# Performance work log

Hardware: AMD Instinct MI355X
Metric: run time of the kernel (lower is better)

## Reference

```python
import jax, jax.numpy as jnp
import numpy as np

B, N, C, H = 4, 2048, 256, 16
D = C // H  # head dim = 16


def setup_inputs() -> dict:
    key = jax.random.key(0)
    k1, k2, k3 = jax.random.split(key, 3)
    x = jax.random.normal(k1, (B, N, C), dtype=jnp.float32)
    w_qkv = jax.random.normal(k2, (C, 3 * C), dtype=jnp.float32) * (C ** -0.5)
    b_qkv = jnp.zeros((3 * C,), dtype=jnp.float32)
    w_proj = jax.random.normal(k3, (C, C), dtype=jnp.float32) * (C ** -0.5)
    b_proj = jnp.zeros((C,), dtype=jnp.float32)
    return {"x": x, "w_qkv": w_qkv, "b_qkv": b_qkv, "w_proj": w_proj, "b_proj": b_proj}


def reference(x, w_qkv, b_qkv, w_proj, b_proj):
    b, n, c = x.shape
    qkv = x @ w_qkv + b_qkv                       # (B, N, 3C)
    qkv = qkv.reshape(b, n, 3, H, D)
    q = jnp.transpose(qkv[:, :, 0], (0, 2, 1, 3))  # (B, H, N, D)
    k = jnp.transpose(qkv[:, :, 1], (0, 2, 1, 3))
    v = jnp.transpose(qkv[:, :, 2], (0, 2, 1, 3))
    # NOTE: the original module applies NO 1/sqrt(d) scaling.
    attn = jnp.einsum('bhqd,bhkd->bhqk', q, k)     # (B, H, N, N)
    attn = jax.nn.softmax(attn, axis=-1)
    out = jnp.einsum('bhqk,bhkd->bhqd', attn, v)   # (B, H, N, D)
    out = jnp.transpose(out, (0, 2, 1, 3)).reshape(b, n, c)
    return out @ w_proj + b_proj
```

## Files before the change

kernel.cpp:

```cpp
#include <hip/hip_runtime.h>
#include <stdint.h>

typedef __attribute__((ext_vector_type(8))) short short8;
typedef __attribute__((ext_vector_type(4))) short short4v;
typedef __attribute__((ext_vector_type(4))) float float4v;
typedef __attribute__((ext_vector_type(16))) float float16v;
typedef __attribute__((ext_vector_type(4))) uint32_t uint4v;

__device__ __forceinline__ short f2bf(float f) {
    union { float f; uint32_t u; } v; v.f = f;
    uint32_t u = v.u;
    uint32_t r = (u + 0x7fffu + ((u >> 16) & 1u)) >> 16;
    return (short)r;
}

#if __has_builtin(__builtin_amdgcn_cvt_pk_bf16_f32)
typedef __bf16 bf16x2_t __attribute__((ext_vector_type(2)));
__device__ __forceinline__ uint32_t cvt_pk2(float a, float b) {
    union { bf16x2_t v; uint32_t u; } c;
    c.v = __builtin_amdgcn_cvt_pk_bf16_f32(a, b);
    return c.u;
}
#else
__device__ __forceinline__ uint32_t cvt_pk2(float a, float b) {
    union { float f; uint32_t u; } x, y; x.f = a; y.f = b;
    return ((x.u + 0x8000u) >> 16) | ((y.u + 0x8000u) & 0xFFFF0000u);
}
#endif

__device__ __forceinline__ void async_ld16(short* lds, const short* g) {
    __builtin_amdgcn_global_load_lds(
        (const __attribute__((address_space(1))) void*)g,
        (__attribute__((address_space(3))) void*)lds, 16, 0, 0);
}


__global__ __launch_bounds__(256) void cvtW_kernel(const float* __restrict__ wqkv,
                                                   const float* __restrict__ wproj,
                                                   const float* __restrict__ x,
                                                   short* __restrict__ outq,
                                                   short* __restrict__ outp,
                                                   short* __restrict__ xb) {
    int gid = blockIdx.x * 256 + threadIdx.x;
    if (gid < 262144) {
        const float* src = x + (size_t)gid * 8;
        float4 f0 = *(const float4*)src;
        float4 f1 = *(const float4*)(src + 4);
        uint4v u; u.x = cvt_pk2(f0.x, f0.y); u.y = cvt_pk2(f0.z, f0.w);
        u.z = cvt_pk2(f1.x, f1.y); u.w = cvt_pk2(f1.z, f1.w);
        *(uint4v*)(xb + (size_t)gid * 8) = u;
    } else {
        int idx = gid - 262144;
        if (idx < 196608) {
            int n = idx >> 8, k = idx & 255;
            outq[idx] = f2bf(wqkv[k * 768 + n]);
        } else {
            int i = idx - 196608;
            int n = i >> 8, k = i & 255;
            outp[i] = f2bf(wproj[k * 256 + n]);
        }
    }
}


template<int TM, int MODE>
__global__ __launch_bounds__(256) void gemm2_kernel(
    const short* __restrict__ A, const short* __restrict__ Bt,
    const float* __restrict__ bias,
    short* __restrict__ outQ, short* __restrict__ outK, short* __restrict__ outV,
    float* __restrict__ outP)
{
    const int K = 256;
    const int MI = TM / 32;
    int tid = threadIdx.x;
    int w = tid >> 6, lane = tid & 63;
    int wr = w >> 1, wc = w & 1;
    int quad = lane >> 4, lc = lane & 15;
    int m0 = blockIdx.x * TM, n0 = blockIdx.y * 128;

    __shared__ __align__(16) short As[TM * 64];
    __shared__ __align__(16) short Bs[128 * 64];

    float4v acc[MI][4];
    #pragma unroll
    for (int i = 0; i < MI; ++i)
        #pragma unroll
        for (int j = 0; j < 4; ++j) acc[i][j] = (float4v){0.f, 0.f, 0.f, 0.f};

    int l8 = lane >> 3, l7 = lane & 7;
    int scol = ((l7 ^ l8) * 8);

    for (int kt = 0; kt < 4; ++kt) {
        int c = kt * 64;
        __syncthreads();
        #pragma unroll
        for (int i = 0; i < TM / 32; ++i) {
            int row = i * 32 + w * 8 + l8;
            async_ld16(&As[row * 64 + l7 * 8],
                       A + (size_t)(m0 + row) * K + c + scol);
        }
        #pragma unroll
        for (int i = 0; i < 4; ++i) {
            int row = i * 32 + w * 8 + l8;
            async_ld16(&Bs[row * 64 + l7 * 8],
                       Bt + (size_t)(n0 + row) * K + c + scol);
        }
        __syncthreads();

        #pragma unroll
        for (int ks = 0; ks < 2; ++ks) {
            short8 af[MI], bf[4];
            #pragma unroll
            for (int i = 0; i < MI; ++i) {
                int r = wr * (TM / 2) + i * 16 + lc;
                af[i] = *(short8*)(&As[r * 64 + (((ks * 4 + quad) ^ (r & 7)) * 8)]);
            }
            #pragma unroll
            for (int j = 0; j < 4; ++j) {
                int r = wc * 64 + j * 16 + lc;
                bf[j] = *(short8*)(&Bs[r * 64 + (((ks * 4 + quad) ^ (r & 7)) * 8)]);
            }
            #pragma unroll
            for (int i = 0; i < MI; ++i)
                #pragma unroll
                for (int j = 0; j < 4; ++j)
                    acc[i][j] = __builtin_amdgcn_mfma_f32_16x16x32_bf16(af[i], bf[j], acc[i][j], 0, 0, 0);
        }
    }

    #pragma unroll
    for (int i = 0; i < MI; ++i) {
        #pragma unroll
        for (int j = 0; j < 4; ++j) {
            int cg = n0 + wc * 64 + j * 16 + lc;
            float bv = bias[cg];
            #pragma unroll
            for (int r = 0; r < 4; ++r) {
                int rg = m0 + wr * (TM / 2) + i * 16 + quad * 4 + r;
                float val = acc[i][j][r] + bv;
                if (MODE == 0) {
                    int sq = cg >> 8, rem = cg & 255, h = rem >> 4, d = rem & 15;
                    int b = rg >> 11, n = rg & 2047;
                    if (sq == 0) val *= 1.4426950408889634f;
                    short* dst = (sq == 0) ? outQ : ((sq == 1) ? outK : outV);
                    dst[((((size_t)b * 16 + h) * 2048 + n) << 4) + d] = f2bf(val);
                } else {
                    outP[(size_t)rg * 256 + cg] = val;
                }
            }
        }
    }
}


__global__ __launch_bounds__(256) void attn_kernel(
    const short* __restrict__ Q, const short* __restrict__ Kp, const short* __restrict__ V,
    short* __restrict__ Out)
{
    const int N = 2048;
    int bh = blockIdx.y;
    int b = bh >> 4, h = bh & 15;
    int tid = threadIdx.x;
    int wave = tid >> 6, lane = tid & 63;
    int m = lane & 31, hi = lane >> 5;
    int qbase = blockIdx.x * 128 + wave * 32;

    const short* Qh = Q + (size_t)bh * N * 16;
    const short* Kh = Kp + (size_t)bh * N * 16;
    const short* Vh = V + (size_t)bh * N * 16;

    __shared__ __align__(16) short Vt[32][264];

    for (int idx = tid; idx < 16 * 264; idx += 256) {
        int row = 16 + idx / 264;
        int col = idx - (row - 16) * 264;
        Vt[row][col] = (row == 16) ? (short)0x3F80 : (short)0;
    }

    short8 qf = *(const short8*)(Qh + (size_t)(qbase + m) * 16 + hi * 8);

    float16v Oacc, zf;
    #pragma unroll
    for (int j = 0; j < 16; ++j) { Oacc[j] = 0.f; zf[j] = 0.f; }

    int sd = tid & 15, sa = tid >> 4;
    int kb = ((sa & 1) << 3) | (((sa >> 1) & 1) << 2) | ((sa >> 2) << 4);

    short4v vpack[4];
    #pragma unroll
    for (int cc = 0; cc < 4; ++cc) {
        const short* vp = Vh + (size_t)(cc * 64 + kb) * 16 + sd;
        vpack[cc].x = vp[0]; vpack[cc].y = vp[16];
        vpack[cc].z = vp[32]; vpack[cc].w = vp[48];
    }

    short8 kf1 = *(const short8*)(Kh + (size_t)m * 16 + hi * 8);
    short8 kf2 = *(const short8*)(Kh + (size_t)(32 + m) * 16 + hi * 8);

    for (int sc = 0; sc < N; sc += 256) {
        __syncthreads();
        #pragma unroll
        for (int cc = 0; cc < 4; ++cc)
            *(short4v*)(&Vt[sd][cc * 64 + sa * 4]) = vpack[cc];
        if (sc + 256 < N) {
            #pragma unroll
            for (int cc = 0; cc < 4; ++cc) {
                const short* vp = Vh + (size_t)(sc + 256 + cc * 64 + kb) * 16 + sd;
                vpack[cc].x = vp[0]; vpack[cc].y = vp[16];
                vpack[cc].z = vp[32]; vpack[cc].w = vp[48];
            }
        }
        __syncthreads();

        #pragma unroll
        for (int it = 0; it < 4; ++it) {
            int c = sc + it * 64;
            int cn = (c + 64) & (N - 1);

            float16v S1 = __builtin_amdgcn_mfma_f32_32x32x16_bf16(kf1, qf, zf, 0, 0, 0);
            float16v S2 = __builtin_amdgcn_mfma_f32_32x32x16_bf16(kf2, qf, zf, 0, 0, 0);

            kf1 = *(const short8*)(Kh + (size_t)(cn + m) * 16 + hi * 8);
            kf2 = *(const short8*)(Kh + (size_t)(cn + 32 + m) * 16 + hi * 8);

            union { uint4v u; short8 s; } pA, pB, pC, pD;
            pA.u = (uint4v){
                cvt_pk2(__builtin_amdgcn_exp2f(S1[0]), __builtin_amdgcn_exp2f(S1[1])),
                cvt_pk2(__builtin_amdgcn_exp2f(S1[2]), __builtin_amdgcn_exp2f(S1[3])),
                cvt_pk2(__builtin_amdgcn_exp2f(S1[4]), __builtin_amdgcn_exp2f(S1[5])),
                cvt_pk2(__builtin_amdgcn_exp2f(S1[6]), __builtin_amdgcn_exp2f(S1[7]))};
            pB.u = (uint4v){
                cvt_pk2(__builtin_amdgcn_exp2f(S1[8]),  __builtin_amdgcn_exp2f(S1[9])),
                cvt_pk2(__builtin_amdgcn_exp2f(S1[10]), __builtin_amdgcn_exp2f(S1[11])),
                cvt_pk2(__builtin_amdgcn_exp2f(S1[12]), __builtin_amdgcn_exp2f(S1[13])),
                cvt_pk2(__builtin_amdgcn_exp2f(S1[14]), __builtin_amdgcn_exp2f(S1[15]))};
            pC.u = (uint4v){
                cvt_pk2(__builtin_amdgcn_exp2f(S2[0]), __builtin_amdgcn_exp2f(S2[1])),
                cvt_pk2(__builtin_amdgcn_exp2f(S2[2]), __builtin_amdgcn_exp2f(S2[3])),
                cvt_pk2(__builtin_amdgcn_exp2f(S2[4]), __builtin_amdgcn_exp2f(S2[5])),
                cvt_pk2(__builtin_amdgcn_exp2f(S2[6]), __builtin_amdgcn_exp2f(S2[7]))};
            pD.u = (uint4v){
                cvt_pk2(__builtin_amdgcn_exp2f(S2[8]),  __builtin_amdgcn_exp2f(S2[9])),
                cvt_pk2(__builtin_amdgcn_exp2f(S2[10]), __builtin_amdgcn_exp2f(S2[11])),
                cvt_pk2(__builtin_amdgcn_exp2f(S2[12]), __builtin_amdgcn_exp2f(S2[13])),
                cvt_pk2(__builtin_amdgcn_exp2f(S2[14]), __builtin_amdgcn_exp2f(S2[15]))};

            #pragma unroll
            for (int p = 0; p < 4; ++p) {
                short8 vf = *(short8*)(&Vt[m][it * 64 + p * 16 + hi * 8]);
                short8 pf = (p == 0) ? pA.s : (p == 1) ? pB.s : (p == 2) ? pC.s : pD.s;
                Oacc = __builtin_amdgcn_mfma_f32_32x32x16_bf16(vf, pf, Oacc, 0, 0, 0);
            }
        }
    }

    float Lq = __shfl(Oacc[8], m, 64);
    float inv = 1.0f / Lq;
    uint32_t o0 = cvt_pk2(Oacc[0] * inv, Oacc[1] * inv);
    uint32_t o1 = cvt_pk2(Oacc[2] * inv, Oacc[3] * inv);
    uint32_t o2 = cvt_pk2(Oacc[4] * inv, Oacc[5] * inv);
    uint32_t o3 = cvt_pk2(Oacc[6] * inv, Oacc[7] * inv);
    short* row = Out + ((size_t)(b * 2048 + qbase + m)) * 256 + h * 16;
    uint2 w0; w0.x = o0; w0.y = o1;
    uint2 w1; w1.x = o2; w1.y = o3;
    *(uint2*)(row + hi * 4) = w0;
    *(uint2*)(row + 8 + hi * 4) = w1;
}


extern "C" void kernel_launch(void* const* d_in, const int* in_sizes, int n_in,
                              void* d_out, int out_size, void* d_ws, size_t ws_size,
                              hipStream_t stream) {
    const float* x      = (const float*)d_in[0];
    const float* w_qkv  = (const float*)d_in[1];
    const float* b_qkv  = (const float*)d_in[2];
    const float* w_proj = (const float*)d_in[3];
    const float* b_proj = (const float*)d_in[4];
    float* out = (float*)d_out;

    short* wqkvT  = (short*)d_ws;
    short* wprojT = wqkvT + 196608;
    short* xb     = wprojT + 65536;
    short* Qb     = xb + 2097152;
    short* Kb     = Qb + 2097152;
    short* Vb     = Kb + 2097152;
    short* Ab     = Vb + 2097152;

    cvtW_kernel<<<2048, 256, 0, stream>>>(w_qkv, w_proj, x, wqkvT, wprojT, xb);

    gemm2_kernel<128, 0><<<dim3(64, 6), 256, 0, stream>>>(xb, wqkvT, b_qkv,
                                                          Qb, Kb, Vb, nullptr);

    attn_kernel<<<dim3(16, 64), 256, 0, stream>>>(Qb, Kb, Vb, Ab);

    gemm2_kernel<64, 1><<<dim3(128, 2), 256, 0, stream>>>(Ab, wprojT, b_proj,
                                                          nullptr, nullptr, nullptr, out);
}
```

Before: 136.2 us.

## Fuse x fp32-to-bf16 conversion into QKV GEMM and tile weight transpose via LDS

The separate pass that converted x to bf16 is removed. The QKV GEMM now loads fp32 x directly, converts it in registers and writes swizzled bf16 into LDS, replacing the async global-to-LDS copy for the A operand. The weight conversion kernel now does a 64x64 tiled transpose through shared memory with coalesced reads and writes, launched as 64 blocks. This saves a global round trip of x and a kernel's worth of memory traffic, at the cost of synchronous loads in the GEMM, and x is re-read in fp32 by each of the 6 column blocks.

```diff
diff --git a/kernel.cpp b/kernel.cpp
--- a/kernel.cpp
+++ b/kernel.cpp
@@ -37,35 +37,43 @@
 
 __global__ __launch_bounds__(256) void cvtW_kernel(const float* __restrict__ wqkv,
                                                    const float* __restrict__ wproj,
-                                                   const float* __restrict__ x,
                                                    short* __restrict__ outq,
-                                                   short* __restrict__ outp,
-                                                   short* __restrict__ xb) {
-    int gid = blockIdx.x * 256 + threadIdx.x;
-    if (gid < 262144) {
-        const float* src = x + (size_t)gid * 8;
-        float4 f0 = *(const float4*)src;
-        float4 f1 = *(const float4*)(src + 4);
-        uint4v u; u.x = cvt_pk2(f0.x, f0.y); u.y = cvt_pk2(f0.z, f0.w);
-        u.z = cvt_pk2(f1.x, f1.y); u.w = cvt_pk2(f1.z, f1.w);
-        *(uint4v*)(xb + (size_t)gid * 8) = u;
+                                                   short* __restrict__ outp) {
+    __shared__ short T[64][66];
+    int t = blockIdx.x;
+    const float* src; short* dst; int srcld, k0, n0;
+    if (t < 48) {
+        k0 = (t & 3) * 64; n0 = (t >> 2) * 64;
+        src = wqkv; srcld = 768; dst = outq;
     } else {
-        int idx = gid - 262144;
-        if (idx < 196608) {
-            int n = idx >> 8, k = idx & 255;
-            outq[idx] = f2bf(wqkv[k * 768 + n]);
-        } else {
-            int i = idx - 196608;
-            int n = i >> 8, k = i & 255;
-            outp[i] = f2bf(wproj[k * 256 + n]);
-        }
-    }
+        int i = t - 48;
+        k0 = (i & 3) * 64; n0 = (i >> 2) * 64;
+        src = wproj; srcld = 256; dst = outp;
+    }
+    int row = threadIdx.x >> 2, seg = threadIdx.x & 3;
+    const float* s = src + (size_t)(k0 + row) * srcld + n0 + seg * 16;
+    float4 f0 = *(const float4*)s;
+    float4 f1 = *(const float4*)(s + 4);
+    float4 f2 = *(const float4*)(s + 8);
+    float4 f3 = *(const float4*)(s + 12);
+    uint32_t* tw = (uint32_t*)&T[row][seg * 16];
+    tw[0] = cvt_pk2(f0.x, f0.y); tw[1] = cvt_pk2(f0.z, f0.w);
+    tw[2] = cvt_pk2(f1.x, f1.y); tw[3] = cvt_pk2(f1.z, f1.w);
+    tw[4] = cvt_pk2(f2.x, f2.y); tw[5] = cvt_pk2(f2.z, f2.w);
+    tw[6] = cvt_pk2(f3.x, f3.y); tw[7] = cvt_pk2(f3.z, f3.w);
+    __syncthreads();
+    short tmp[16] __attribute__((aligned(16)));
+    #pragma unroll
+    for (int j = 0; j < 16; ++j) tmp[j] = T[seg * 16 + j][row];
+    short* d = dst + (size_t)(n0 + row) * 256 + k0 + seg * 16;
+    *(short8*)d       = *(short8*)&tmp[0];
+    *(short8*)(d + 8) = *(short8*)&tmp[8];
 }
 
 
 template<int TM, int MODE>
 __global__ __launch_bounds__(256) void gemm2_kernel(
-    const short* __restrict__ A, const short* __restrict__ Bt,
+    const void* __restrict__ Ap, const short* __restrict__ Bt,
     const float* __restrict__ bias,
     short* __restrict__ outQ, short* __restrict__ outK, short* __restrict__ outV,
     float* __restrict__ outP)
@@ -93,11 +101,26 @@
     for (int kt = 0; kt < 4; ++kt) {
         int c = kt * 64;
         __syncthreads();
-        #pragma unroll
-        for (int i = 0; i < TM / 32; ++i) {
-            int row = i * 32 + w * 8 + l8;
-            async_ld16(&As[row * 64 + l7 * 8],
-                       A + (size_t)(m0 + row) * K + c + scol);
+        if (MODE == 0) {
+            const float* Af = (const float*)Ap;
+            #pragma unroll
+            for (int i = 0; i < 4; ++i) {
+                int row = i * 32 + (tid >> 3);
+                int seg = tid & 7;
+                const float* src = Af + (size_t)(m0 + row) * K + c + seg * 8;
+                float4 f0 = *(const float4*)src;
+                float4 f1 = *(const float4*)(src + 4);
+                uint4v u; u.x = cvt_pk2(f0.x, f0.y); u.y = cvt_pk2(f0.z, f0.w);
+                u.z = cvt_pk2(f1.x, f1.y); u.w = cvt_pk2(f1.z, f1.w);
+                *(uint4v*)(&As[row * 64 + ((seg ^ (row & 7)) * 8)]) = u;
+            }
+        } else {
+            #pragma unroll
+            for (int i = 0; i < TM / 32; ++i) {
+                int row = i * 32 + w * 8 + l8;
+                async_ld16(&As[row * 64 + l7 * 8],
+                           (const short*)Ap + (size_t)(m0 + row) * K + c + scol);
+            }
         }
         #pragma unroll
         for (int i = 0; i < 4; ++i) {
@@ -280,15 +303,14 @@
 
     short* wqkvT  = (short*)d_ws;
     short* wprojT = wqkvT + 196608;
-    short* xb     = wprojT + 65536;
-    short* Qb     = xb + 2097152;
+    short* Qb     = wprojT + 65536;
     short* Kb     = Qb + 2097152;
     short* Vb     = Kb + 2097152;
     short* Ab     = Vb + 2097152;
 
-    cvtW_kernel<<<2048, 256, 0, stream>>>(w_qkv, w_proj, x, wqkvT, wprojT, xb);
-
-    gemm2_kernel<128, 0><<<dim3(64, 6), 256, 0, stream>>>(xb, wqkvT, b_qkv,
+    cvtW_kernel<<<64, 256, 0, stream>>>(w_qkv, w_proj, wqkvT, wprojT);
+
+    gemm2_kernel<128, 0><<<dim3(64, 6), 256, 0, stream>>>(x, wqkvT, b_qkv,
                                                           Qb, Kb, Vb, nullptr);
 
     attn_kernel<<<dim3(16, 64), 256, 0, stream>>>(Qb, Kb, Vb, Ab);
```

Result: no change. 135.1 us (-0.8%).
